# Kernel tuning notes

Measured on AMD Instinct MI355X. Metric: run time of the kernel, lower is better.

## Reference

```python
import jax, jax.numpy as jnp
import numpy as np

EPS = 1e-8  # matches init eps


def setup_inputs() -> dict:
    key = jax.random.key(0)
    ks = jax.random.split(key, 6)
    B, LA, LB, Dh, P = 2, 512, 512, 1024, 64
    return {
        "h_a": jax.random.normal(ks[0], (B, LA, Dh), dtype=jnp.float32),
        "h_b": jax.random.normal(ks[1], (B, LB, Dh), dtype=jnp.float32),
        "Wa": jax.random.normal(ks[2], (Dh, P), dtype=jnp.float32) * 0.02,
        "ba": jax.random.normal(ks[3], (P,), dtype=jnp.float32) * 0.02,
        "Wb": jax.random.normal(ks[4], (Dh, P), dtype=jnp.float32) * 0.02,
        "bb": jax.random.normal(ks[5], (P,), dtype=jnp.float32) * 0.02,
    }


def reference(h_a, h_b, Wa, ba, Wb, bb):
    # Project + exact GELU (torch default)
    z_a = jax.nn.gelu(h_a @ Wa + ba, approximate=False)  # [B,LA,P]
    z_b = jax.nn.gelu(h_b @ Wb + bb, approximate=False)  # [B,LB,P]
    B, LA, P = z_a.shape
    LB = z_b.shape[1]
    # Channel-first broadcasts: [B,P,LA,LB]
    za = jnp.transpose(z_a, (0, 2, 1))[:, :, :, None]  # [B,P,LA,1]
    zb = jnp.transpose(z_b, (0, 2, 1))[:, :, None, :]  # [B,P,1,LB]
    za_e = jnp.broadcast_to(za, (B, P, LA, LB))
    zb_e = jnp.broadcast_to(zb, (B, P, LA, LB))
    diff = jnp.abs(za_e - zb_e)
    prod = za_e * zb_e
    # cosine similarity channel, computed from per-residue stats (no D-expanded tensor)
    dot = jnp.einsum("bip,bjp->bij", z_a, z_b)[:, None]  # [B,1,LA,LB]
    na = jnp.sqrt(jnp.sum(z_a * z_a, axis=-1) + EPS)  # [B,LA]
    nb = jnp.sqrt(jnp.sum(z_b * z_b, axis=-1) + EPS)  # [B,LB]
    sim = dot / (na[:, None, :, None] * nb[:, None, None, :])
    # channel order matches torch cat([z_a, z_b, diff, prod, sim], -1).permute(0,3,1,2)
    return jnp.concatenate([za_e, zb_e, diff, prod, sim], axis=1)  # [B,4P+1,LA,LB]
```

## Files before the change

### kernel.cpp

```cpp
#include <hip/hip_runtime.h>
#include <math.h>

#define B_    2
#define LA_   512
#define LB_   512
#define DH_   1024
#define P_    64
#define NCH_  257
#define EPS_  1e-8f
#define CH_   ((size_t)LA_ * LB_)

#define SIMBLK_  256
#define WBLK_    1792
#define NQ_      ((size_t)512 * CH_ / 4)
#define WSTRIDE_ ((size_t)WBLK_ * 256)

__global__ __launch_bounds__(256) void proj_gelu_kernel(
    const float* __restrict__ h_a, const float* __restrict__ Wa,
    const float* __restrict__ ba,
    const float* __restrict__ h_b, const float* __restrict__ Wb,
    const float* __restrict__ bb,
    float* __restrict__ zat,
    float* __restrict__ zbt,
    float* __restrict__ rna,
    float* __restrict__ rnb)
{
    __shared__ __align__(16) float hs[DH_];
    __shared__ __align__(16) float partial[256 * 4];

    const int side = blockIdx.x >> 10;
    const int row  = blockIdx.x & 1023;
    const int b    = row >> 9;
    const int i    = row & 511;
    const int tid  = threadIdx.x;

    const float* h    = side ? h_b : h_a;
    const float* W    = side ? Wb  : Wa;
    const float* bias = side ? bb  : ba;
    float* z  = side ? zbt : zat;
    float* rn = side ? rnb : rna;

    ((float4*)hs)[tid] = ((const float4*)(h + (size_t)row * DH_))[tid];
    __syncthreads();

    const int pg = (tid & 15) * 4;
    const int q  = tid >> 4;
    const float* Wq = W + (size_t)(q * 64) * P_ + pg;
    float4 acc = make_float4(0.f, 0.f, 0.f, 0.f);
    #pragma unroll 8
    for (int k = 0; k < 64; ++k) {
        const float  hv = hs[q * 64 + k];
        const float4 w  = *(const float4*)(Wq + (size_t)k * P_);
        acc.x = fmaf(hv, w.x, acc.x);
        acc.y = fmaf(hv, w.y, acc.y);
        acc.z = fmaf(hv, w.z, acc.z);
        acc.w = fmaf(hv, w.w, acc.w);
    }
    *(float4*)(partial + tid * 4) = acc;
    __syncthreads();

    if (tid < 64) {
        float v = partial[tid];
        #pragma unroll
        for (int qq = 1; qq < 16; ++qq)
            v += partial[qq * 64 + tid];
        v += bias[tid];
        float g = 0.5f * v * (1.f + erff(v * 0.70710678118654752f));

        z[((size_t)(b * P_ + tid)) * 512 + i] = g;

        float s = g * g;
        #pragma unroll
        for (int off = 32; off > 0; off >>= 1)
            s += __shfl_down(s, off, 64);
        if (tid == 0)
            rn[row] = 1.f / sqrtf(s + EPS_);
    }
}

__global__ __launch_bounds__(256) void map_kernel(
    const float* __restrict__ zat,
    const float* __restrict__ zbt,
    const float* __restrict__ rna,
    const float* __restrict__ rnb,
    float* __restrict__ out)
{
    const int tid = threadIdx.x;
    const int bid = blockIdx.x;

    if (bid >= SIMBLK_) {
        const int wid = bid - SIMBLK_;
        size_t q = (size_t)wid * 256 + tid;
        #pragma unroll 2
        for (; q < NQ_; q += WSTRIDE_) {
            const int plane = (int)(q >> 16);
            const int b     = plane >> 8;
            const int ch    = plane & 255;
            const int t     = ch >> 6;
            const int p     = ch & 63;
            const int w4    = (int)(q & 65535);
            const int i     = w4 >> 7;
            const int j     = (w4 & 127) << 2;

            const size_t zoff = ((size_t)((b << 6) + p)) << 9;
            const float  a    = zat[zoff + i];
            const float4 zb   = *(const float4*)(zbt + zoff + j);

            float4 v;
            if (t == 0)       v = make_float4(a, a, a, a);
            else if (t == 1)  v = zb;
            else if (t == 2)  v = make_float4(fabsf(a - zb.x), fabsf(a - zb.y),
                                              fabsf(a - zb.z), fabsf(a - zb.w));
            else              v = make_float4(a * zb.x, a * zb.y,
                                              a * zb.z, a * zb.w);

            float* op = out + (((size_t)(b * NCH_ + ch)) << 18) + ((size_t)w4 << 2);
            *(float4*)op = v;
        }
    } else {
        __shared__ __align__(16) float zas[P_ * 16];

        const int s  = bid;
        const int b  = s >> 7;
        const int r  = s & 127;
        const int i0 = (r >> 2) * 16;
        const int j0 = (r & 3) * 128;

        {
            const int p  = tid >> 2;
            const int i4 = (tid & 3) * 4;
            *(float4*)(zas + p * 16 + i4) =
                *(const float4*)(zat + (size_t)(b * P_ + p) * 512 + i0 + i4);
        }
        __syncthreads();

        const int rr = tid >> 7;
        const int j  = j0 + (tid & 127);

        float acc[8];
        #pragma unroll
        for (int u = 0; u < 8; ++u) acc[u] = 0.f;

        for (int p = 0; p < P_; ++p) {
            const float zb = zbt[(size_t)(b * P_ + p) * 512 + j];
            #pragma unroll
            for (int u = 0; u < 8; ++u)
                acc[u] = fmaf(zas[p * 16 + rr * 8 + u], zb, acc[u]);
        }

        const float rbj = rnb[b * 512 + j];
        float* plane = out + (size_t)(b * NCH_ + 256) * CH_;
        #pragma unroll
        for (int u = 0; u < 8; ++u) {
            const int i = i0 + rr * 8 + u;
            plane[(size_t)i * LB_ + j] = acc[u] * rna[b * 512 + i] * rbj;
        }
    }
}

extern "C" void kernel_launch(void* const* d_in, const int* in_sizes, int n_in,
                              void* d_out, int out_size, void* d_ws, size_t ws_size,
                              hipStream_t stream)
{
    const float* h_a = (const float*)d_in[0];
    const float* h_b = (const float*)d_in[1];
    const float* Wa  = (const float*)d_in[2];
    const float* ba  = (const float*)d_in[3];
    const float* Wb  = (const float*)d_in[4];
    const float* bb  = (const float*)d_in[5];
    float* out = (float*)d_out;

    float* ws  = (float*)d_ws;
    float* zat = ws;
    float* zbt = zat + (size_t)B_ * P_ * LA_;
    float* rna = zbt + (size_t)B_ * P_ * LB_;
    float* rnb = rna + (size_t)B_ * LA_;

    proj_gelu_kernel<<<2 * B_ * LA_, 256, 0, stream>>>(
        h_a, Wa, ba, h_b, Wb, bb, zat, zbt, rna, rnb);
    map_kernel<<<dim3(SIMBLK_ + WBLK_), 256, 0, stream>>>(
        zat, zbt, rna, rnb, out);
}
```

Before: 545.9 us.

## Tile broadcast-channel writes per plane quarter with register-held zb row

Replaces the grid-stride loop over flattened float4 outputs with one block per (batch, channel, quarter-plane). Each thread loads its zb float4 once, and the block stages a column of zat values in shared memory. Each block then streams 128 rows of stores with a channel-uniform branch. This removes per-element index decoding, redundant zat/zbt loads and warp divergence on the channel type, at the cost of a much larger grid (2048 writer blocks) instead of a persistent-style loop.

```diff
diff --git a/kernel.cpp b/kernel.cpp
--- a/kernel.cpp
+++ b/kernel.cpp
@@ -11,9 +11,8 @@
 #define CH_   ((size_t)LA_ * LB_)
 
 #define SIMBLK_  256
-#define WBLK_    1792
-#define NQ_      ((size_t)512 * CH_ / 4)
-#define WSTRIDE_ ((size_t)WBLK_ * 256)
+#define WQ_      4
+#define QROWS_   (LA_ / WQ_)
 
 __global__ __launch_bounds__(256) void proj_gelu_kernel(
     const float* __restrict__ h_a, const float* __restrict__ Wa,
@@ -89,33 +88,58 @@
     const int bid = blockIdx.x;
 
     if (bid >= SIMBLK_) {
-        const int wid = bid - SIMBLK_;
-        size_t q = (size_t)wid * 256 + tid;
-        #pragma unroll 2
-        for (; q < NQ_; q += WSTRIDE_) {
-            const int plane = (int)(q >> 16);
-            const int b     = plane >> 8;
-            const int ch    = plane & 255;
-            const int t     = ch >> 6;
-            const int p     = ch & 63;
-            const int w4    = (int)(q & 65535);
-            const int i     = w4 >> 7;
-            const int j     = (w4 & 127) << 2;
-
-            const size_t zoff = ((size_t)((b << 6) + p)) << 9;
-            const float  a    = zat[zoff + i];
-            const float4 zb   = *(const float4*)(zbt + zoff + j);
-
-            float4 v;
-            if (t == 0)       v = make_float4(a, a, a, a);
-            else if (t == 1)  v = zb;
-            else if (t == 2)  v = make_float4(fabsf(a - zb.x), fabsf(a - zb.y),
-                                              fabsf(a - zb.z), fabsf(a - zb.w));
-            else              v = make_float4(a * zb.x, a * zb.y,
-                                              a * zb.z, a * zb.w);
-
-            float* op = out + (((size_t)(b * NCH_ + ch)) << 18) + ((size_t)w4 << 2);
-            *(float4*)op = v;
+        __shared__ __align__(16) float zacol[QROWS_];
+
+        const int w       = bid - SIMBLK_;
+        const int plane   = w >> 2;
+        const int quarter = w & 3;
+        const int b       = plane >> 8;
+        const int ch      = plane & 255;
+        const int t       = ch >> 6;
+        const int p       = ch & 63;
+        const int i0      = quarter * QROWS_;
+
+        const size_t zoff = ((size_t)(b * P_ + p)) << 9;
+
+        const int jj = (tid & 127) * 4;
+        const float4 zbv = *(const float4*)(zbt + zoff + jj);
+        if (tid < 32)
+            ((float4*)zacol)[tid] = ((const float4*)(zat + zoff + i0))[tid];
+        __syncthreads();
+
+        const int half = tid >> 7;
+        float* op = out + (((size_t)(b * NCH_ + ch)) << 18)
+                        + (size_t)(i0 + half) * LB_ + jj;
+
+        if (t == 1) {
+            #pragma unroll 8
+            for (int it = 0; it < QROWS_ / 2; ++it) {
+                *(float4*)op = zbv;
+                op += 2 * LB_;
+            }
+        } else if (t == 0) {
+            #pragma unroll 8
+            for (int it = 0; it < QROWS_ / 2; ++it) {
+                const float a = zacol[2 * it + half];
+                *(float4*)op = make_float4(a, a, a, a);
+                op += 2 * LB_;
+            }
+        } else if (t == 2) {
+            #pragma unroll 8
+            for (int it = 0; it < QROWS_ / 2; ++it) {
+                const float a = zacol[2 * it + half];
+                *(float4*)op = make_float4(fabsf(a - zbv.x), fabsf(a - zbv.y),
+                                           fabsf(a - zbv.z), fabsf(a - zbv.w));
+                op += 2 * LB_;
+            }
+        } else {
+            #pragma unroll 8
+            for (int it = 0; it < QROWS_ / 2; ++it) {
+                const float a = zacol[2 * it + half];
+                *(float4*)op = make_float4(a * zbv.x, a * zbv.y,
+                                           a * zbv.z, a * zbv.w);
+                op += 2 * LB_;
+            }
         }
     } else {
         __shared__ __align__(16) float zas[P_ * 16];
@@ -178,6 +202,6 @@
 
     proj_gelu_kernel<<<2 * B_ * LA_, 256, 0, stream>>>(
         h_a, Wa, ba, h_b, Wb, bb, zat, zbt, rna, rnb);
-    map_kernel<<<dim3(SIMBLK_ + WBLK_), 256, 0, stream>>>(
+    map_kernel<<<dim3(SIMBLK_ + B_ * 256 * WQ_), 256, 0, stream>>>(
         zat, zbt, rna, rnb, out);
 }
```

Measured after the change: 556.7 us. Within noise of the previous version (+2.0%).
